# Kernel optimization log

Hardware: AMD Instinct MI355X
Metric: run time of the kernel (lower is better)

The kernel has to match this reference:

```python
import jax, jax.numpy as jnp
import numpy as np

N_NODES = 50000
N_EDGES = 800000
D_IN = 96
D_HID = 96
D_OUT = 4


def _glorot(key, shape):
    lim = float(np.sqrt(6.0 / (shape[0] + shape[1])))
    return jax.random.uniform(key, shape, jnp.float32, -lim, lim)


def setup_inputs() -> dict:
    key = jax.random.key(0)
    ks = jax.random.split(key, 8)
    x = jax.random.normal(ks[0], (N_NODES, D_IN), jnp.float32)
    edge_index = jax.random.randint(ks[1], (2, N_EDGES), 0, N_NODES, jnp.int64)
    return {
        'x': x,
        'edge_index': edge_index,
        'W0': _glorot(ks[2], (D_IN, D_HID)), 'b0': jnp.zeros((D_HID,), jnp.float32),
        'W1': _glorot(ks[3], (D_HID, D_HID)), 'b1': jnp.zeros((D_HID,), jnp.float32),
        'W2': _glorot(ks[4], (D_HID, D_HID)), 'b2': jnp.zeros((D_HID,), jnp.float32),
        'Wfc': _glorot(ks[5], (D_HID, D_OUT)), 'bfc': jnp.zeros((D_OUT,), jnp.float32),
    }


def _gcn_conv(x, src, dst, W, b, n):
    # GCNConv: linear transform, add self-loops, symmetric degree norm, scatter-add.
    h = x @ W                                   # [N, D]
    loops = jnp.arange(n, dtype=src.dtype)
    s = jnp.concatenate([src, loops])           # [E+N]
    d = jnp.concatenate([dst, loops])
    deg = jax.ops.segment_sum(jnp.ones_like(d, dtype=h.dtype), d, num_segments=n)
    dinv = jnp.where(deg > 0, jax.lax.rsqrt(deg), 0.0)
    norm = dinv[s] * dinv[d]                    # [E+N]
    msgs = h[s] * norm[:, None]                 # gather + scale
    out = jax.ops.segment_sum(msgs, d, num_segments=n)  # scatter-add
    return out + b


def reference(x, edge_index, W0, b0, W1, b1, W2, b2, Wfc, bfc):
    src, dst = edge_index[0], edge_index[1]
    n = x.shape[0]
    h = jax.nn.relu(_gcn_conv(x, src, dst, W0, b0, n))   # dropout = identity (eval)
    h = jax.nn.relu(_gcn_conv(h, src, dst, W1, b1, n))
    h = jax.nn.relu(_gcn_conv(h, src, dst, W2, b2, n))
    return h @ Wfc + bfc
```

## Files before the change

kernel.cpp:

```cpp
#include <hip/hip_runtime.h>

typedef __bf16 bf16x8 __attribute__((ext_vector_type(8)));
typedef float  f32x4  __attribute__((ext_vector_type(4)));
typedef float  f32x8  __attribute__((ext_vector_type(8)));
typedef unsigned short ushort;
typedef ushort us8 __attribute__((ext_vector_type(8)));

constexpr int N_NODES = 50000;
constexpr int N_EDGES = 800000;
constexpr int D = 96;
constexpr int SLOTS = 64;
constexpr int GE = (N_EDGES + 255) / 256;
constexpr int WBLK = (3 * 9216 + 255) / 256;

__global__ __launch_bounds__(256) void k_countfill(const int* __restrict__ src,
                                                   const int* __restrict__ dst,
                                                   int* __restrict__ cnt,
                                                   int* __restrict__ csr,
                                                   const float* __restrict__ W0,
                                                   const float* __restrict__ W1,
                                                   const float* __restrict__ W2,
                                                   ushort* __restrict__ Wt) {
    const int b = blockIdx.x;
    if (b < GE) {
        int e = b * 256 + threadIdx.x;
        if (e < N_EDGES) {
            int d = dst[e];
            int rank = atomicAdd(&cnt[d], 1);
            csr[d * SLOTS + rank] = src[e];
        }
    } else {
        int i = (b - GE) * 256 + threadIdx.x;
        if (i < 3 * 9216) {
            int m = i / 9216, li = i - m * 9216;
            const float* W = (m == 0) ? W0 : (m == 1) ? W1 : W2;
            int k = li / 96, c = li - k * 96;
            union { __bf16 bb; ushort u; } cv;
            cv.bb = (__bf16)W[li];
            Wt[m * 9216 + c * 96 + k] = cv.u;
        }
    }
}

template<bool FP32IN>
__global__ __launch_bounds__(256) void k_gemm_mfma(const void* Xv, const ushort* __restrict__ Wt,
                                                   ushort* __restrict__ Y, int nrows) {
    __shared__ ushort sX[64 * 96];
    __shared__ ushort sW[96 * 96];
    const int tid = threadIdx.x;
    const int rowbase = blockIdx.x * 64;

    for (int i = tid; i < 96 * 96 / 8; i += 256)
        ((uint4*)sW)[i] = ((const uint4*)Wt)[i];

    if (FP32IN) {
        const float* X = (const float*)Xv;
        for (int i = tid; i < 64 * 24; i += 256) {
            int r = i / 24, c4 = i % 24;
            int gr = rowbase + r;
            float4 v = make_float4(0.f, 0.f, 0.f, 0.f);
            if (gr < nrows) v = ((const float4*)(X + (size_t)gr * 96))[c4];
            union { __bf16 b; ushort u; } cx, cy, cz, cw;
            cx.b = (__bf16)v.x; cy.b = (__bf16)v.y; cz.b = (__bf16)v.z; cw.b = (__bf16)v.w;
            ushort* p = sX + r * 96 + c4 * 4;
            p[0] = cx.u; p[1] = cy.u; p[2] = cz.u; p[3] = cw.u;
        }
    } else {
        const ushort* X = (const ushort*)Xv;
        for (int i = tid; i < 64 * 12; i += 256) {
            int r = i / 12, c8 = i % 12;
            int gr = rowbase + r;
            uint4 v = make_uint4(0, 0, 0, 0);
            if (gr < nrows) v = ((const uint4*)(X + (size_t)gr * 96))[c8];
            ((uint4*)(sX + r * 96))[c8] = v;
        }
    }
    __syncthreads();

    const int wv = tid >> 6, lane = tid & 63, quad = lane >> 4, l16 = lane & 15;
    f32x4 acc[6];
#pragma unroll
    for (int t = 0; t < 6; ++t) acc[t] = (f32x4){0.f, 0.f, 0.f, 0.f};

    const ushort* ax = sX + (wv * 16 + l16) * 96 + quad * 8;
#pragma unroll
    for (int s = 0; s < 3; ++s) {
        bf16x8 a = *(const bf16x8*)(ax + s * 32);
#pragma unroll
        for (int t = 0; t < 6; ++t) {
            bf16x8 b = *(const bf16x8*)(sW + (t * 16 + l16) * 96 + s * 32 + quad * 8);
            acc[t] = __builtin_amdgcn_mfma_f32_16x16x32_bf16(a, b, acc[t], 0, 0, 0);
        }
    }
    const int r0 = rowbase + wv * 16 + quad * 4;
#pragma unroll
    for (int t = 0; t < 6; ++t) {
#pragma unroll
        for (int g = 0; g < 4; ++g) {
            int r = r0 + g;
            if (r < nrows) {
                union { __bf16 b; ushort u; } cv;
                cv.b = (__bf16)acc[t][g];
                Y[(size_t)r * 96 + t * 16 + l16] = cv.u;
            }
        }
    }
}

__device__ inline f32x8 bf8_to_f32(us8 u) {
    f32x8 r;
#pragma unroll
    for (int i = 0; i < 8; ++i) r[i] = __uint_as_float(((unsigned int)u[i]) << 16);
    return r;
}

__device__ inline float deg_inv(const int* cnt, int n) {
    return rsqrtf((float)(cnt[n] + 1));
}

template<int MODE>
__global__ __launch_bounds__(192) void k_agg(const ushort* __restrict__ A,
                                             const int* __restrict__ cnt,
                                             const int* __restrict__ csr,
                                             const float* __restrict__ bias,
                                             ushort* __restrict__ Hout,
                                             float* __restrict__ out4,
                                             const float* __restrict__ Wfc,
                                             const float* __restrict__ bfc) {
    __shared__ float sWfc[384];
    __shared__ float red[16][12][4];
    const int tid = threadIdx.x;
    if (MODE == 1) {
        for (int i = tid; i < 384; i += 192) sWfc[i] = Wfc[i];
        __syncthreads();
    }
    const int g = tid / 12, c = tid % 12;
    const int n = blockIdx.x * 16 + g;

    const int deg = cnt[n];
    const float dn = rsqrtf((float)(deg + 1));
    us8 a0 = *(const us8*)(A + (size_t)n * 96 + c * 8);
    f32x8 acc = bf8_to_f32(a0) * (dn * dn);

    const int* ecs = csr + n * SLOTS;
    int j = 0;
    for (; j + 4 <= deg; j += 4) {
        const int s0 = ecs[j + 0];
        const int s1 = ecs[j + 1];
        const int s2 = ecs[j + 2];
        const int s3 = ecs[j + 3];
        const float w0 = deg_inv(cnt, s0) * dn;
        const float w1 = deg_inv(cnt, s1) * dn;
        const float w2 = deg_inv(cnt, s2) * dn;
        const float w3 = deg_inv(cnt, s3) * dn;
        const us8 u0 = *(const us8*)(A + (size_t)s0 * 96 + c * 8);
        const us8 u1 = *(const us8*)(A + (size_t)s1 * 96 + c * 8);
        const us8 u2 = *(const us8*)(A + (size_t)s2 * 96 + c * 8);
        const us8 u3 = *(const us8*)(A + (size_t)s3 * 96 + c * 8);
        acc += bf8_to_f32(u0) * w0;
        acc += bf8_to_f32(u1) * w1;
        acc += bf8_to_f32(u2) * w2;
        acc += bf8_to_f32(u3) * w3;
    }
    for (; j < deg; ++j) {
        const int s = ecs[j];
        const float w = deg_inv(cnt, s) * dn;
        const us8 u = *(const us8*)(A + (size_t)s * 96 + c * 8);
        acc += bf8_to_f32(u) * w;
    }
#pragma unroll
    for (int f = 0; f < 8; ++f) acc[f] = fmaxf(acc[f] + bias[c * 8 + f], 0.0f);

    if (MODE == 0) {
        us8 o;
#pragma unroll
        for (int f = 0; f < 8; ++f) {
            union { __bf16 b; ushort u; } cv;
            cv.b = (__bf16)acc[f];
            o[f] = cv.u;
        }
        *(us8*)(Hout + (size_t)n * 96 + c * 8) = o;
    } else {
        float p0 = 0.f, p1 = 0.f, p2 = 0.f, p3 = 0.f;
#pragma unroll
        for (int f = 0; f < 8; ++f) {
            const float* wr = sWfc + (c * 8 + f) * 4;
            p0 += acc[f] * wr[0];
            p1 += acc[f] * wr[1];
            p2 += acc[f] * wr[2];
            p3 += acc[f] * wr[3];
        }
        red[g][c][0] = p0; red[g][c][1] = p1; red[g][c][2] = p2; red[g][c][3] = p3;
        __syncthreads();
        if (tid < 64) {
            const int gg = tid >> 2, jj = tid & 3;
            float s = bfc[jj];
#pragma unroll
            for (int cc = 0; cc < 12; ++cc) s += red[gg][cc][jj];
            out4[(size_t)(blockIdx.x * 16 + gg) * 4 + jj] = s;
        }
    }
}

extern "C" void kernel_launch(void* const* d_in, const int* in_sizes, int n_in,
                              void* d_out, int out_size, void* d_ws, size_t ws_size,
                              hipStream_t stream) {
    const float* x   = (const float*)d_in[0];
    const int*   ei  = (const int*)d_in[1];
    const int*   src = ei;
    const int*   dst = ei + N_EDGES;
    const float* W0  = (const float*)d_in[2];
    const float* b0  = (const float*)d_in[3];
    const float* W1  = (const float*)d_in[4];
    const float* b1  = (const float*)d_in[5];
    const float* W2  = (const float*)d_in[6];
    const float* b2  = (const float*)d_in[7];
    const float* Wfc = (const float*)d_in[8];
    const float* bfc = (const float*)d_in[9];
    float* out = (float*)d_out;

    char* w = (char*)d_ws;
    int*    csr = (int*)w;                w += ((size_t)N_NODES * SLOTS * 4 + 15) & ~15ULL;
    int*    cnt = (int*)w;                w += ((size_t)N_NODES * 4 + 15) & ~15ULL;
    ushort* Wt  = (ushort*)w;             w += ((size_t)3 * 9216 * 2 + 15) & ~15ULL;
    ushort* H   = (ushort*)w;             w += ((size_t)N_NODES * D * 2 + 15) & ~15ULL;
    ushort* G   = (ushort*)w;

    const int B256 = 256;
    const int gMf  = (N_NODES + 63) / 64;
    const int gAgg = N_NODES / 16;

    hipMemsetAsync(cnt, 0, (size_t)N_NODES * 4, stream);
    hipLaunchKernelGGL(k_countfill, dim3(GE + WBLK), dim3(B256), 0, stream,
                       src, dst, cnt, csr, W0, W1, W2, Wt);

    hipLaunchKernelGGL((k_gemm_mfma<true>),  dim3(gMf), dim3(B256), 0, stream,
                       (const void*)x, Wt, H, N_NODES);
    hipLaunchKernelGGL((k_agg<0>), dim3(gAgg), dim3(192), 0, stream,
                       H, cnt, csr, b0, G, (float*)nullptr,
                       (const float*)nullptr, (const float*)nullptr);
    hipLaunchKernelGGL((k_gemm_mfma<false>), dim3(gMf), dim3(B256), 0, stream,
                       (const void*)G, Wt + 9216, H, N_NODES);
    hipLaunchKernelGGL((k_agg<0>), dim3(gAgg), dim3(192), 0, stream,
                       H, cnt, csr, b1, G, (float*)nullptr,
                       (const float*)nullptr, (const float*)nullptr);
    hipLaunchKernelGGL((k_gemm_mfma<false>), dim3(gMf), dim3(B256), 0, stream,
                       (const void*)G, Wt + 2 * 9216, H, N_NODES);
    hipLaunchKernelGGL((k_agg<1>), dim3(gAgg), dim3(192), 0, stream,
                       H, cnt, csr, b2, (ushort*)nullptr, out, Wfc, bfc);
}
```

Baseline: 248.8 us.

## Use channel-major feature layout, packed CSR with precomputed norms, split fc

Feature matrices are stored channel-chunk-major ([12][N][8]) so each aggregation block handles one 8-wide channel chunk for 256 nodes. Each thread loads 8 neighbours per iteration, and all blocks working on a chunk share a compact 800 KB region, which should improve cache reuse of gathers. CSR entries now pack a 16-bit source index with an fp16 source-degree normalisation, computed in a separate fill pass after counting. This removes the per-edge cnt lookup and rsqrt inside aggregation. The final fc moves to its own kernel reading an fp32 intermediate, adding one kernel launch and an extra global round trip.

```diff
diff --git a/kernel.cpp b/kernel.cpp
--- a/kernel.cpp
+++ b/kernel.cpp
@@ -8,41 +8,55 @@
 
 constexpr int N_NODES = 50000;
 constexpr int N_EDGES = 800000;
-constexpr int D = 96;
 constexpr int SLOTS = 64;
-constexpr int GE = (N_EDGES + 255) / 256;
-constexpr int WBLK = (3 * 9216 + 255) / 256;
-
-__global__ __launch_bounds__(256) void k_countfill(const int* __restrict__ src,
-                                                   const int* __restrict__ dst,
-                                                   int* __restrict__ cnt,
-                                                   int* __restrict__ csr,
-                                                   const float* __restrict__ W0,
-                                                   const float* __restrict__ W1,
-                                                   const float* __restrict__ W2,
-                                                   ushort* __restrict__ Wt) {
+constexpr int NCH = 12;
+constexpr int NB = (N_NODES + 255) / 256;
+constexpr int GE = N_EDGES / 256;
+constexpr int WBLK = (3 * 9216) / 256;
+
+__device__ inline float h16f(ushort u) {
+    union { _Float16 h; ushort u; } cv; cv.u = u; return (float)cv.h;
+}
+__device__ inline ushort f16b(float f) {
+    union { _Float16 h; ushort u; } cv; cv.h = (_Float16)f; return cv.u;
+}
+__device__ inline ushort bf16b(float f) {
+    union { __bf16 b; ushort u; } cv; cv.b = (__bf16)f; return cv.u;
+}
+
+__global__ __launch_bounds__(256) void k_count(const int* __restrict__ dst,
+                                               int* __restrict__ cnt,
+                                               ushort* __restrict__ rank,
+                                               const float* __restrict__ W0,
+                                               const float* __restrict__ W1,
+                                               const float* __restrict__ W2,
+                                               ushort* __restrict__ Wt) {
     const int b = blockIdx.x;
     if (b < GE) {
         int e = b * 256 + threadIdx.x;
-        if (e < N_EDGES) {
-            int d = dst[e];
-            int rank = atomicAdd(&cnt[d], 1);
-            csr[d * SLOTS + rank] = src[e];
-        }
+        rank[e] = (ushort)atomicAdd(&cnt[dst[e]], 1);
     } else {
         int i = (b - GE) * 256 + threadIdx.x;
-        if (i < 3 * 9216) {
-            int m = i / 9216, li = i - m * 9216;
-            const float* W = (m == 0) ? W0 : (m == 1) ? W1 : W2;
-            int k = li / 96, c = li - k * 96;
-            union { __bf16 bb; ushort u; } cv;
-            cv.bb = (__bf16)W[li];
-            Wt[m * 9216 + c * 96 + k] = cv.u;
-        }
-    }
-}
-
-template<bool FP32IN>
+        int m = i / 9216, li = i - m * 9216;
+        const float* W = (m == 0) ? W0 : (m == 1) ? W1 : W2;
+        int k = li / 96, c = li - k * 96;
+        Wt[m * 9216 + c * 96 + k] = bf16b(W[li]);
+    }
+}
+
+__global__ __launch_bounds__(256) void k_fill(const int* __restrict__ src,
+                                              const int* __restrict__ dst,
+                                              const int* __restrict__ cnt,
+                                              const ushort* __restrict__ rank,
+                                              unsigned int* __restrict__ csr) {
+    int e = blockIdx.x * 256 + threadIdx.x;
+    int s = src[e], d = dst[e];
+    float hs = rsqrtf((float)(cnt[s] + 1));
+    unsigned int entry = (unsigned int)(ushort)s | ((unsigned int)f16b(hs) << 16);
+    csr[(size_t)d * SLOTS + rank[e]] = entry;
+}
+
+template<int IN>
 __global__ __launch_bounds__(256) void k_gemm_mfma(const void* Xv, const ushort* __restrict__ Wt,
                                                    ushort* __restrict__ Y, int nrows) {
     __shared__ ushort sX[64 * 96];
@@ -53,26 +67,24 @@
     for (int i = tid; i < 96 * 96 / 8; i += 256)
         ((uint4*)sW)[i] = ((const uint4*)Wt)[i];
 
-    if (FP32IN) {
+    if (IN == 0) {
         const float* X = (const float*)Xv;
         for (int i = tid; i < 64 * 24; i += 256) {
             int r = i / 24, c4 = i % 24;
             int gr = rowbase + r;
             float4 v = make_float4(0.f, 0.f, 0.f, 0.f);
             if (gr < nrows) v = ((const float4*)(X + (size_t)gr * 96))[c4];
-            union { __bf16 b; ushort u; } cx, cy, cz, cw;
-            cx.b = (__bf16)v.x; cy.b = (__bf16)v.y; cz.b = (__bf16)v.z; cw.b = (__bf16)v.w;
             ushort* p = sX + r * 96 + c4 * 4;
-            p[0] = cx.u; p[1] = cy.u; p[2] = cz.u; p[3] = cw.u;
+            p[0] = bf16b(v.x); p[1] = bf16b(v.y); p[2] = bf16b(v.z); p[3] = bf16b(v.w);
         }
     } else {
         const ushort* X = (const ushort*)Xv;
-        for (int i = tid; i < 64 * 12; i += 256) {
-            int r = i / 12, c8 = i % 12;
-            int gr = rowbase + r;
-            uint4 v = make_uint4(0, 0, 0, 0);
-            if (gr < nrows) v = ((const uint4*)(X + (size_t)gr * 96))[c8];
-            ((uint4*)(sX + r * 96))[c8] = v;
+        for (int i = tid; i < NCH * 64; i += 256) {
+            int c = i >> 6, rr = i & 63;
+            int gr = rowbase + rr;
+            us8 v = (us8){0, 0, 0, 0, 0, 0, 0, 0};
+            if (gr < nrows) v = *(const us8*)(X + ((size_t)c * N_NODES + gr) * 8);
+            *(us8*)(sX + rr * 96 + c * 8) = v;
         }
     }
     __syncthreads();
@@ -95,14 +107,12 @@
     const int r0 = rowbase + wv * 16 + quad * 4;
 #pragma unroll
     for (int t = 0; t < 6; ++t) {
+        const int col = t * 16 + l16;
+        const int cc = col >> 3, ff = col & 7;
 #pragma unroll
         for (int g = 0; g < 4; ++g) {
             int r = r0 + g;
-            if (r < nrows) {
-                union { __bf16 b; ushort u; } cv;
-                cv.b = (__bf16)acc[t][g];
-                Y[(size_t)r * 96 + t * 16 + l16] = cv.u;
-            }
+            if (r < nrows) Y[((size_t)cc * N_NODES + r) * 8 + ff] = bf16b(acc[t][g]);
         }
     }
 }
@@ -114,92 +124,85 @@
     return r;
 }
 
-__device__ inline float deg_inv(const int* cnt, int n) {
-    return rsqrtf((float)(cnt[n] + 1));
-}
-
-template<int MODE>
-__global__ __launch_bounds__(192) void k_agg(const ushort* __restrict__ A,
-                                             const int* __restrict__ cnt,
-                                             const int* __restrict__ csr,
-                                             const float* __restrict__ bias,
-                                             ushort* __restrict__ Hout,
-                                             float* __restrict__ out4,
-                                             const float* __restrict__ Wfc,
-                                             const float* __restrict__ bfc) {
-    __shared__ float sWfc[384];
-    __shared__ float red[16][12][4];
-    const int tid = threadIdx.x;
-    if (MODE == 1) {
-        for (int i = tid; i < 384; i += 192) sWfc[i] = Wfc[i];
-        __syncthreads();
-    }
-    const int g = tid / 12, c = tid % 12;
-    const int n = blockIdx.x * 16 + g;
+template<int OUT>
+__global__ __launch_bounds__(256) void k_aggT(const ushort* __restrict__ A,
+                                              const int* __restrict__ cnt,
+                                              const unsigned int* __restrict__ csr,
+                                              const float* __restrict__ bias,
+                                              ushort* __restrict__ O16,
+                                              float* __restrict__ O32) {
+    const int c = blockIdx.x % NCH;
+    const int n = (blockIdx.x / NCH) * 256 + threadIdx.x;
+    if (n >= N_NODES) return;
 
     const int deg = cnt[n];
     const float dn = rsqrtf((float)(deg + 1));
-    us8 a0 = *(const us8*)(A + (size_t)n * 96 + c * 8);
-    f32x8 acc = bf8_to_f32(a0) * (dn * dn);
-
-    const int* ecs = csr + n * SLOTS;
+    const ushort* Ac = A + (size_t)c * N_NODES * 8;
+
+    f32x8 acc = bf8_to_f32(*(const us8*)(Ac + (size_t)n * 8)) * (dn * dn);
+
+    const unsigned int* row = csr + (size_t)n * SLOTS;
     int j = 0;
-    for (; j + 4 <= deg; j += 4) {
-        const int s0 = ecs[j + 0];
-        const int s1 = ecs[j + 1];
-        const int s2 = ecs[j + 2];
-        const int s3 = ecs[j + 3];
-        const float w0 = deg_inv(cnt, s0) * dn;
-        const float w1 = deg_inv(cnt, s1) * dn;
-        const float w2 = deg_inv(cnt, s2) * dn;
-        const float w3 = deg_inv(cnt, s3) * dn;
-        const us8 u0 = *(const us8*)(A + (size_t)s0 * 96 + c * 8);
-        const us8 u1 = *(const us8*)(A + (size_t)s1 * 96 + c * 8);
-        const us8 u2 = *(const us8*)(A + (size_t)s2 * 96 + c * 8);
-        const us8 u3 = *(const us8*)(A + (size_t)s3 * 96 + c * 8);
-        acc += bf8_to_f32(u0) * w0;
-        acc += bf8_to_f32(u1) * w1;
-        acc += bf8_to_f32(u2) * w2;
-        acc += bf8_to_f32(u3) * w3;
+    for (; j + 8 <= deg; j += 8) {
+        uint4 q0 = *(const uint4*)(row + j);
+        uint4 q1 = *(const uint4*)(row + j + 4);
+        unsigned int es[8] = {q0.x, q0.y, q0.z, q0.w, q1.x, q1.y, q1.z, q1.w};
+        us8 u[8];
+#pragma unroll
+        for (int k = 0; k < 8; ++k)
+            u[k] = *(const us8*)(Ac + (size_t)(es[k] & 0xFFFFu) * 8);
+#pragma unroll
+        for (int k = 0; k < 8; ++k) {
+            const float w = h16f((ushort)(es[k] >> 16)) * dn;
+            acc += bf8_to_f32(u[k]) * w;
+        }
     }
     for (; j < deg; ++j) {
-        const int s = ecs[j];
-        const float w = deg_inv(cnt, s) * dn;
-        const us8 u = *(const us8*)(A + (size_t)s * 96 + c * 8);
+        const unsigned int e = row[j];
+        const float w = h16f((ushort)(e >> 16)) * dn;
+        const us8 u = *(const us8*)(Ac + (size_t)(e & 0xFFFFu) * 8);
         acc += bf8_to_f32(u) * w;
     }
 #pragma unroll
     for (int f = 0; f < 8; ++f) acc[f] = fmaxf(acc[f] + bias[c * 8 + f], 0.0f);
 
-    if (MODE == 0) {
+    if (OUT == 0) {
         us8 o;
 #pragma unroll
+        for (int f = 0; f < 8; ++f) o[f] = bf16b(acc[f]);
+        *(us8*)(O16 + ((size_t)c * N_NODES + n) * 8) = o;
+    } else {
+        *(f32x8*)(O32 + ((size_t)c * N_NODES + n) * 8) = acc;
+    }
+}
+
+__global__ __launch_bounds__(256) void k_fc(const float* __restrict__ H,
+                                            const float* __restrict__ Wfc,
+                                            const float* __restrict__ bfc,
+                                            float4* __restrict__ out) {
+    __shared__ float sW[384];
+    __shared__ float sb[4];
+    const int tid = threadIdx.x;
+    for (int i = tid; i < 384; i += 256) sW[i] = Wfc[i];
+    if (tid < 4) sb[tid] = bfc[tid];
+    __syncthreads();
+
+    const int n = blockIdx.x * 256 + tid;
+    if (n >= N_NODES) return;
+    float acc[4] = {sb[0], sb[1], sb[2], sb[3]};
+#pragma unroll
+    for (int c = 0; c < NCH; ++c) {
+        f32x8 h = *(const f32x8*)(H + ((size_t)c * N_NODES + n) * 8);
+#pragma unroll
         for (int f = 0; f < 8; ++f) {
-            union { __bf16 b; ushort u; } cv;
-            cv.b = (__bf16)acc[f];
-            o[f] = cv.u;
-        }
-        *(us8*)(Hout + (size_t)n * 96 + c * 8) = o;
-    } else {
-        float p0 = 0.f, p1 = 0.f, p2 = 0.f, p3 = 0.f;
-#pragma unroll
-        for (int f = 0; f < 8; ++f) {
-            const float* wr = sWfc + (c * 8 + f) * 4;
-            p0 += acc[f] * wr[0];
-            p1 += acc[f] * wr[1];
-            p2 += acc[f] * wr[2];
-            p3 += acc[f] * wr[3];
-        }
-        red[g][c][0] = p0; red[g][c][1] = p1; red[g][c][2] = p2; red[g][c][3] = p3;
-        __syncthreads();
-        if (tid < 64) {
-            const int gg = tid >> 2, jj = tid & 3;
-            float s = bfc[jj];
-#pragma unroll
-            for (int cc = 0; cc < 12; ++cc) s += red[gg][cc][jj];
-            out4[(size_t)(blockIdx.x * 16 + gg) * 4 + jj] = s;
-        }
-    }
+            const float* wr = sW + (c * 8 + f) * 4;
+            acc[0] += h[f] * wr[0];
+            acc[1] += h[f] * wr[1];
+            acc[2] += h[f] * wr[2];
+            acc[3] += h[f] * wr[3];
+        }
+    }
+    out[n] = make_float4(acc[0], acc[1], acc[2], acc[3]);
 }
 
 extern "C" void kernel_launch(void* const* d_in, const int* in_sizes, int n_in,
@@ -220,32 +223,34 @@
     float* out = (float*)d_out;
 
     char* w = (char*)d_ws;
-    int*    csr = (int*)w;                w += ((size_t)N_NODES * SLOTS * 4 + 15) & ~15ULL;
-    int*    cnt = (int*)w;                w += ((size_t)N_NODES * 4 + 15) & ~15ULL;
-    ushort* Wt  = (ushort*)w;             w += ((size_t)3 * 9216 * 2 + 15) & ~15ULL;
-    ushort* H   = (ushort*)w;             w += ((size_t)N_NODES * D * 2 + 15) & ~15ULL;
-    ushort* G   = (ushort*)w;
-
-    const int B256 = 256;
+    unsigned int* csr = (unsigned int*)w;  w += ((size_t)N_NODES * SLOTS * 4 + 15) & ~15ULL;
+    int*    cnt  = (int*)w;                w += ((size_t)N_NODES * 4 + 15) & ~15ULL;
+    ushort* rank = (ushort*)w;             w += ((size_t)N_EDGES * 2 + 15) & ~15ULL;
+    ushort* Wt   = (ushort*)w;             w += ((size_t)3 * 9216 * 2 + 15) & ~15ULL;
+    ushort* H    = (ushort*)w;             w += ((size_t)N_NODES * 96 * 2 + 15) & ~15ULL;
+    ushort* G    = (ushort*)w;             w += ((size_t)N_NODES * 96 * 2 + 15) & ~15ULL;
+    float*  H3   = (float*)w;
+
     const int gMf  = (N_NODES + 63) / 64;
-    const int gAgg = N_NODES / 16;
+    const int gAgg = NB * NCH;
 
     hipMemsetAsync(cnt, 0, (size_t)N_NODES * 4, stream);
-    hipLaunchKernelGGL(k_countfill, dim3(GE + WBLK), dim3(B256), 0, stream,
-                       src, dst, cnt, csr, W0, W1, W2, Wt);
-
-    hipLaunchKernelGGL((k_gemm_mfma<true>),  dim3(gMf), dim3(B256), 0, stream,
+    hipLaunchKernelGGL(k_count, dim3(GE + WBLK), dim3(256), 0, stream,
+                       dst, cnt, rank, W0, W1, W2, Wt);
+    hipLaunchKernelGGL(k_fill,  dim3(GE), dim3(256), 0, stream,
+                       src, dst, cnt, rank, csr);
+
+    hipLaunchKernelGGL((k_gemm_mfma<0>), dim3(gMf), dim3(256), 0, stream,
                        (const void*)x, Wt, H, N_NODES);
-    hipLaunchKernelGGL((k_agg<0>), dim3(gAgg), dim3(192), 0, stream,
-                       H, cnt, csr, b0, G, (float*)nullptr,
-                       (const float*)nullptr, (const float*)nullptr);
-    hipLaunchKernelGGL((k_gemm_mfma<false>), dim3(gMf), dim3(B256), 0, stream,
+    hipLaunchKernelGGL((k_aggT<0>), dim3(gAgg), dim3(256), 0, stream,
+                       H, cnt, csr, b0, G, (float*)nullptr);
+    hipLaunchKernelGGL((k_gemm_mfma<1>), dim3(gMf), dim3(256), 0, stream,
                        (const void*)G, Wt + 9216, H, N_NODES);
-    hipLaunchKernelGGL((k_agg<0>), dim3(gAgg), dim3(192), 0, stream,
-                       H, cnt, csr, b1, G, (float*)nullptr,
-                       (const float*)nullptr, (const float*)nullptr);
-    hipLaunchKernelGGL((k_gemm_mfma<false>), dim3(gMf), dim3(B256), 0, stream,
+    hipLaunchKernelGGL((k_aggT<0>), dim3(gAgg), dim3(256), 0, stream,
+                       H, cnt, csr, b1, G, (float*)nullptr);
+    hipLaunchKernelGGL((k_gemm_mfma<1>), dim3(gMf), dim3(256), 0, stream,
                        (const void*)G, Wt + 2 * 9216, H, N_NODES);
-    hipLaunchKernelGGL((k_agg<1>), dim3(gAgg), dim3(192), 0, stream,
-                       H, cnt, csr, b2, (ushort*)nullptr, out, Wfc, bfc);
-}
+    hipLaunchKernelGGL((k_aggT<1>), dim3(gAgg), dim3(256), 0, stream,
+                       H, cnt, csr, b2, (ushort*)nullptr, H3);
+    hipLaunchKernelGGL(k_fc, dim3(NB), dim3(256), 0, stream, H3, Wfc, bfc, (float4*)out);
+}
```

New measurement: 374.7 us. 50.6% more time.

## Pack source index and fp16 source norm into CSR entries via two-pass build

Applied to the files above, without the earlier changes.

CSR construction is split into a count pass that records each edge's rank and a fill pass that writes entries after all degrees are known. Each entry packs the 16-bit source index with the fp16 rsqrt of the source degree. The aggregation kernels read four entries with one 128-bit load and no longer gather cnt[s] per edge. This adds an extra launch and a rank array, and relies on node ids fitting in 16 bits and on fp16 precision for the norm.

```diff
diff --git a/kernel.cpp b/kernel.cpp
--- a/kernel.cpp
+++ b/kernel.cpp
@@ -8,41 +8,53 @@
 
 constexpr int N_NODES = 50000;
 constexpr int N_EDGES = 800000;
-constexpr int D = 96;
 constexpr int SLOTS = 64;
-constexpr int GE = (N_EDGES + 255) / 256;
-constexpr int WBLK = (3 * 9216 + 255) / 256;
-
-__global__ __launch_bounds__(256) void k_countfill(const int* __restrict__ src,
-                                                   const int* __restrict__ dst,
-                                                   int* __restrict__ cnt,
-                                                   int* __restrict__ csr,
-                                                   const float* __restrict__ W0,
-                                                   const float* __restrict__ W1,
-                                                   const float* __restrict__ W2,
-                                                   ushort* __restrict__ Wt) {
+constexpr int GE = N_EDGES / 256;
+constexpr int WBLK = (3 * 9216) / 256;
+
+__device__ inline float h16f(ushort u) {
+    union { _Float16 h; ushort u; } cv; cv.u = u; return (float)cv.h;
+}
+__device__ inline ushort f16b(float f) {
+    union { _Float16 h; ushort u; } cv; cv.h = (_Float16)f; return cv.u;
+}
+__device__ inline ushort bf16b(float f) {
+    union { __bf16 b; ushort u; } cv; cv.b = (__bf16)f; return cv.u;
+}
+
+__global__ __launch_bounds__(256) void k_count(const int* __restrict__ dst,
+                                               int* __restrict__ cnt,
+                                               ushort* __restrict__ rank,
+                                               const float* __restrict__ W0,
+                                               const float* __restrict__ W1,
+                                               const float* __restrict__ W2,
+                                               ushort* __restrict__ Wt) {
     const int b = blockIdx.x;
     if (b < GE) {
         int e = b * 256 + threadIdx.x;
-        if (e < N_EDGES) {
-            int d = dst[e];
-            int rank = atomicAdd(&cnt[d], 1);
-            csr[d * SLOTS + rank] = src[e];
-        }
+        rank[e] = (ushort)atomicAdd(&cnt[dst[e]], 1);
     } else {
         int i = (b - GE) * 256 + threadIdx.x;
-        if (i < 3 * 9216) {
-            int m = i / 9216, li = i - m * 9216;
-            const float* W = (m == 0) ? W0 : (m == 1) ? W1 : W2;
-            int k = li / 96, c = li - k * 96;
-            union { __bf16 bb; ushort u; } cv;
-            cv.bb = (__bf16)W[li];
-            Wt[m * 9216 + c * 96 + k] = cv.u;
-        }
-    }
-}
-
-template<bool FP32IN>
+        int m = i / 9216, li = i - m * 9216;
+        const float* W = (m == 0) ? W0 : (m == 1) ? W1 : W2;
+        int k = li / 96, c = li - k * 96;
+        Wt[m * 9216 + c * 96 + k] = bf16b(W[li]);
+    }
+}
+
+__global__ __launch_bounds__(256) void k_fill(const int* __restrict__ src,
+                                              const int* __restrict__ dst,
+                                              const int* __restrict__ cnt,
+                                              const ushort* __restrict__ rank,
+                                              unsigned int* __restrict__ csr) {
+    int e = blockIdx.x * 256 + threadIdx.x;
+    int s = src[e], d = dst[e];
+    float hs = rsqrtf((float)(cnt[s] + 1));
+    unsigned int entry = (unsigned int)(ushort)s | ((unsigned int)f16b(hs) << 16);
+    csr[(size_t)d * SLOTS + rank[e]] = entry;
+}
+
+template<int IN>
 __global__ __launch_bounds__(256) void k_gemm_mfma(const void* Xv, const ushort* __restrict__ Wt,
                                                    ushort* __restrict__ Y, int nrows) {
     __shared__ ushort sX[64 * 96];
@@ -53,17 +65,15 @@
     for (int i = tid; i < 96 * 96 / 8; i += 256)
         ((uint4*)sW)[i] = ((const uint4*)Wt)[i];
 
-    if (FP32IN) {
+    if (IN == 0) {
         const float* X = (const float*)Xv;
         for (int i = tid; i < 64 * 24; i += 256) {
             int r = i / 24, c4 = i % 24;
             int gr = rowbase + r;
             float4 v = make_float4(0.f, 0.f, 0.f, 0.f);
             if (gr < nrows) v = ((const float4*)(X + (size_t)gr * 96))[c4];
-            union { __bf16 b; ushort u; } cx, cy, cz, cw;
-            cx.b = (__bf16)v.x; cy.b = (__bf16)v.y; cz.b = (__bf16)v.z; cw.b = (__bf16)v.w;
             ushort* p = sX + r * 96 + c4 * 4;
-            p[0] = cx.u; p[1] = cy.u; p[2] = cz.u; p[3] = cw.u;
+            p[0] = bf16b(v.x); p[1] = bf16b(v.y); p[2] = bf16b(v.z); p[3] = bf16b(v.w);
         }
     } else {
         const ushort* X = (const ushort*)Xv;
@@ -98,11 +108,7 @@
 #pragma unroll
         for (int g = 0; g < 4; ++g) {
             int r = r0 + g;
-            if (r < nrows) {
-                union { __bf16 b; ushort u; } cv;
-                cv.b = (__bf16)acc[t][g];
-                Y[(size_t)r * 96 + t * 16 + l16] = cv.u;
-            }
+            if (r < nrows) Y[(size_t)r * 96 + t * 16 + l16] = bf16b(acc[t][g]);
         }
     }
 }
@@ -112,16 +118,12 @@
 #pragma unroll
     for (int i = 0; i < 8; ++i) r[i] = __uint_as_float(((unsigned int)u[i]) << 16);
     return r;
-}
-
-__device__ inline float deg_inv(const int* cnt, int n) {
-    return rsqrtf((float)(cnt[n] + 1));
 }
 
 template<int MODE>
 __global__ __launch_bounds__(192) void k_agg(const ushort* __restrict__ A,
                                              const int* __restrict__ cnt,
-                                             const int* __restrict__ csr,
+                                             const unsigned int* __restrict__ csr,
                                              const float* __restrict__ bias,
                                              ushort* __restrict__ Hout,
                                              float* __restrict__ out4,
@@ -142,30 +144,23 @@
     us8 a0 = *(const us8*)(A + (size_t)n * 96 + c * 8);
     f32x8 acc = bf8_to_f32(a0) * (dn * dn);
 
-    const int* ecs = csr + n * SLOTS;
+    const unsigned int* row = csr + (size_t)n * SLOTS;
     int j = 0;
     for (; j + 4 <= deg; j += 4) {
-        const int s0 = ecs[j + 0];
-        const int s1 = ecs[j + 1];
-        const int s2 = ecs[j + 2];
-        const int s3 = ecs[j + 3];
-        const float w0 = deg_inv(cnt, s0) * dn;
-        const float w1 = deg_inv(cnt, s1) * dn;
-        const float w2 = deg_inv(cnt, s2) * dn;
-        const float w3 = deg_inv(cnt, s3) * dn;
-        const us8 u0 = *(const us8*)(A + (size_t)s0 * 96 + c * 8);
-        const us8 u1 = *(const us8*)(A + (size_t)s1 * 96 + c * 8);
-        const us8 u2 = *(const us8*)(A + (size_t)s2 * 96 + c * 8);
-        const us8 u3 = *(const us8*)(A + (size_t)s3 * 96 + c * 8);
-        acc += bf8_to_f32(u0) * w0;
-        acc += bf8_to_f32(u1) * w1;
-        acc += bf8_to_f32(u2) * w2;
-        acc += bf8_to_f32(u3) * w3;
+        const uint4 q = *(const uint4*)(row + j);
+        const us8 u0 = *(const us8*)(A + (size_t)(q.x & 0xFFFFu) * 96 + c * 8);
+        const us8 u1 = *(const us8*)(A + (size_t)(q.y & 0xFFFFu) * 96 + c * 8);
+        const us8 u2 = *(const us8*)(A + (size_t)(q.z & 0xFFFFu) * 96 + c * 8);
+        const us8 u3 = *(const us8*)(A + (size_t)(q.w & 0xFFFFu) * 96 + c * 8);
+        acc += bf8_to_f32(u0) * (h16f((ushort)(q.x >> 16)) * dn);
+        acc += bf8_to_f32(u1) * (h16f((ushort)(q.y >> 16)) * dn);
+        acc += bf8_to_f32(u2) * (h16f((ushort)(q.z >> 16)) * dn);
+        acc += bf8_to_f32(u3) * (h16f((ushort)(q.w >> 16)) * dn);
     }
     for (; j < deg; ++j) {
-        const int s = ecs[j];
-        const float w = deg_inv(cnt, s) * dn;
-        const us8 u = *(const us8*)(A + (size_t)s * 96 + c * 8);
+        const unsigned int e = row[j];
+        const float w = h16f((ushort)(e >> 16)) * dn;
+        const us8 u = *(const us8*)(A + (size_t)(e & 0xFFFFu) * 96 + c * 8);
         acc += bf8_to_f32(u) * w;
     }
 #pragma unroll
@@ -174,11 +169,7 @@
     if (MODE == 0) {
         us8 o;
 #pragma unroll
-        for (int f = 0; f < 8; ++f) {
-            union { __bf16 b; ushort u; } cv;
-            cv.b = (__bf16)acc[f];
-            o[f] = cv.u;
-        }
+        for (int f = 0; f < 8; ++f) o[f] = bf16b(acc[f]);
         *(us8*)(Hout + (size_t)n * 96 + c * 8) = o;
     } else {
         float p0 = 0.f, p1 = 0.f, p2 = 0.f, p3 = 0.f;
@@ -220,31 +211,33 @@
     float* out = (float*)d_out;
 
     char* w = (char*)d_ws;
-    int*    csr = (int*)w;                w += ((size_t)N_NODES * SLOTS * 4 + 15) & ~15ULL;
-    int*    cnt = (int*)w;                w += ((size_t)N_NODES * 4 + 15) & ~15ULL;
-    ushort* Wt  = (ushort*)w;             w += ((size_t)3 * 9216 * 2 + 15) & ~15ULL;
-    ushort* H   = (ushort*)w;             w += ((size_t)N_NODES * D * 2 + 15) & ~15ULL;
-    ushort* G   = (ushort*)w;
-
-    const int B256 = 256;
+    unsigned int* csr = (unsigned int*)w;  w += ((size_t)N_NODES * SLOTS * 4 + 15) & ~15ULL;
+    int*    cnt  = (int*)w;                w += ((size_t)N_NODES * 4 + 15) & ~15ULL;
+    ushort* rank = (ushort*)w;             w += ((size_t)N_EDGES * 2 + 15) & ~15ULL;
+    ushort* Wt   = (ushort*)w;             w += ((size_t)3 * 9216 * 2 + 15) & ~15ULL;
+    ushort* H    = (ushort*)w;             w += ((size_t)N_NODES * 96 * 2 + 15) & ~15ULL;
+    ushort* G    = (ushort*)w;
+
     const int gMf  = (N_NODES + 63) / 64;
     const int gAgg = N_NODES / 16;
 
     hipMemsetAsync(cnt, 0, (size_t)N_NODES * 4, stream);
-    hipLaunchKernelGGL(k_countfill, dim3(GE + WBLK), dim3(B256), 0, stream,
-                       src, dst, cnt, csr, W0, W1, W2, Wt);
-
-    hipLaunchKernelGGL((k_gemm_mfma<true>),  dim3(gMf), dim3(B256), 0, stream,
+    hipLaunchKernelGGL(k_count, dim3(GE + WBLK), dim3(256), 0, stream,
+                       dst, cnt, rank, W0, W1, W2, Wt);
+    hipLaunchKernelGGL(k_fill,  dim3(GE), dim3(256), 0, stream,
+                       src, dst, cnt, rank, csr);
+
+    hipLaunchKernelGGL((k_gemm_mfma<0>), dim3(gMf), dim3(256), 0, stream,
                        (const void*)x, Wt, H, N_NODES);
     hipLaunchKernelGGL((k_agg<0>), dim3(gAgg), dim3(192), 0, stream,
                        H, cnt, csr, b0, G, (float*)nullptr,
                        (const float*)nullptr, (const float*)nullptr);
-    hipLaunchKernelGGL((k_gemm_mfma<false>), dim3(gMf), dim3(B256), 0, stream,
+    hipLaunchKernelGGL((k_gemm_mfma<1>), dim3(gMf), dim3(256), 0, stream,
                        (const void*)G, Wt + 9216, H, N_NODES);
     hipLaunchKernelGGL((k_agg<0>), dim3(gAgg), dim3(192), 0, stream,
                        H, cnt, csr, b1, G, (float*)nullptr,
                        (const float*)nullptr, (const float*)nullptr);
-    hipLaunchKernelGGL((k_gemm_mfma<false>), dim3(gMf), dim3(B256), 0, stream,
+    hipLaunchKernelGGL((k_gemm_mfma<1>), dim3(gMf), dim3(256), 0, stream,
                        (const void*)G, Wt + 2 * 9216, H, N_NODES);
     hipLaunchKernelGGL((k_agg<1>), dim3(gAgg), dim3(192), 0, stream,
                        H, cnt, csr, b2, (ushort*)nullptr, out, Wfc, bfc);
```

New measurement: 243.6 us. 1.02x faster.
